# Kernel optimization log

Measured on AMD Instinct MI355X. Metric: run time of the kernel, lower is better.

The kernel has to match this reference:

```python
import jax, jax.numpy as jnp
import numpy as np

N_OBS = 8_000_000
N_CAM = 2_000
N_PTS = 1_000_000


def _rotate_quat(points, qt):
    """Rotate points by unit quaternion qt[...,:4]=(w,x,y,z), then translate by qt[...,4:7]."""
    q = qt[..., :4]
    q = q / jnp.linalg.norm(q, axis=-1, keepdims=True)
    w = q[..., :1]          # [N,1]
    v = q[..., 1:4]         # [N,3]
    # p' = p + 2*v x (v x p + w*p)
    t = jnp.cross(v, points) + w * points
    rotated = points + 2.0 * jnp.cross(v, t)
    return rotated + qt[..., 4:7]


def _project(points, camera_params):
    p = _rotate_quat(points, camera_params[..., :7])          # [N,3]
    proj = -p[..., :2] / p[..., 2:3]                          # perspective divide, [N,2]
    f = camera_params[..., 7:8]
    k1 = camera_params[..., 8:9]
    k2 = camera_params[..., 9:10]
    n = jnp.sum(proj * proj, axis=-1, keepdims=True)          # [N,1]
    r = 1.0 + k1 * n + k2 * n * n                             # radial distortion
    return proj * r * f


def setup_inputs() -> dict:
    key = jax.random.key(0)
    k1, k2, k3, k4, k5 = jax.random.split(key, 5)
    camera_params = jax.random.normal(k1, (N_CAM, 10), dtype=jnp.float32)
    # push translation z away from zero so the perspective divide is well-conditioned
    camera_params = camera_params.at[:, 6].add(5.0)
    points_3d = jax.random.normal(k2, (N_PTS, 3), dtype=jnp.float32)
    points_2d = jax.random.normal(k3, (N_OBS, 2), dtype=jnp.float32)
    camera_indices = jax.random.randint(k4, (N_OBS,), 0, N_CAM, dtype=jnp.int32)
    point_indices = jax.random.randint(k5, (N_OBS,), 0, N_PTS, dtype=jnp.int32)
    return {
        "points_2d": points_2d,
        "camera_indices": camera_indices,
        "point_indices": point_indices,
        "camera_params": camera_params,
        "points_3d": points_3d,
    }


def reference(points_2d, camera_indices, point_indices, camera_params, points_3d):
    pts = points_3d[point_indices]           # gather [N,3]
    cams = camera_params[camera_indices]     # gather [N,10]
    points_proj = _project(pts, cams)        # [N,2]
    return points_proj - points_2d
```

## Files before the change

### kernel.cpp

```cpp
#include <hip/hip_runtime.h>


__device__ __forceinline__ float2 project_one(
    int ci, int pi,
    const float* __restrict__ cams,
    const float* __restrict__ pts,
    float2 obs)
{
    const float2* c2 = reinterpret_cast<const float2*>(cams + (size_t)ci * 10);
    float2 c01 = c2[0];
    float2 c23 = c2[1];
    float2 c45 = c2[2];
    float2 c67 = c2[3];
    float2 c89 = c2[4];

    const float* p = pts + (size_t)pi * 3;
    double px = (double)p[0], py = (double)p[1], pz = (double)p[2];

    double qw = (double)c01.x, qx = (double)c01.y;
    double qy = (double)c23.x, qz = (double)c23.y;

    double nrm2 = qw * qw + qx * qx + qy * qy + qz * qz;
    double s = 1.0 / sqrt(nrm2);
    double w  = qw * s;
    double vx = qx * s, vy = qy * s, vz = qz * s;

    double tx = (vy * pz - vz * py) + w * px;
    double ty = (vz * px - vx * pz) + w * py;
    double tz = (vx * py - vy * px) + w * pz;

    double X = (px + 2.0 * (vy * tz - vz * ty)) + (double)c45.x;
    double Y = (py + 2.0 * (vz * tx - vx * tz)) + (double)c45.y;
    double Z = (pz + 2.0 * (vx * ty - vy * tx)) + (double)c67.x;

    double rz  = 1.0 / Z;
    double prx = -X * rz;
    double pry = -Y * rz;

    double f  = (double)c67.y;
    double k1 = (double)c89.x, k2 = (double)c89.y;

    double nn = prx * prx + pry * pry;
    double r  = 1.0 + k1 * nn + k2 * nn * nn;
    double rf = r * f;

    float2 o;
    o.x = (float)(prx * rf - (double)obs.x);
    o.y = (float)(pry * rf - (double)obs.y);
    return o;
}

__global__ __launch_bounds__(256) void reproj_kernel(
    const float2* __restrict__ p2d,
    const int*    __restrict__ cam_idx,
    const int*    __restrict__ pt_idx,
    const float*  __restrict__ cams,
    const float*  __restrict__ pts,
    float2*       __restrict__ out,
    int n)
{
    int t = blockIdx.x * blockDim.x + threadIdx.x;
    int i = t * 2;
    if (i + 1 < n) {
        int2 ci = *reinterpret_cast<const int2*>(cam_idx + i);
        int2 pi = *reinterpret_cast<const int2*>(pt_idx + i);
        float4 ob = *reinterpret_cast<const float4*>(p2d + i);
        float2 o0 = project_one(ci.x, pi.x, cams, pts, make_float2(ob.x, ob.y));
        float2 o1 = project_one(ci.y, pi.y, cams, pts, make_float2(ob.z, ob.w));
        float4 ov = make_float4(o0.x, o0.y, o1.x, o1.y);
        *reinterpret_cast<float4*>(out + i) = ov;
    } else if (i < n) {
        int ci = cam_idx[i];
        int pi = pt_idx[i];
        float2 ob = p2d[i];
        out[i] = project_one(ci, pi, cams, pts, ob);
    }
}

extern "C" void kernel_launch(void* const* d_in, const int* in_sizes, int n_in,
                              void* d_out, int out_size, void* d_ws, size_t ws_size,
                              hipStream_t stream) {
    const float2* p2d     = (const float2*)d_in[0];
    const int*    cam_idx = (const int*)d_in[1];
    const int*    pt_idx  = (const int*)d_in[2];
    const float*  cams    = (const float*)d_in[3];
    const float*  pts     = (const float*)d_in[4];
    float2*       out     = (float2*)d_out;

    int n = in_sizes[1];

    int threads = 256;
    int elems_per_block = threads * 2;
    int blocks = (n + elems_per_block - 1) / elems_per_block;

    reproj_kernel<<<blocks, threads, 0, stream>>>(p2d, cam_idx, pt_idx, cams, pts, out, n);
}
```

Before: 142.2 us.

## Stage camera table in LDS, repack points to float4, use nontemporal streams

Each 1024-thread block copies the whole 80 KB camera table into shared memory, and the camera gathers then read from LDS. A separate pre-kernel repacks the 3-float points into 16-byte float4 entries in the workspace, so each point gather becomes one vector load. Streaming index, observation and output accesses use nontemporal loads and stores. The trade-off is an extra repack kernel pass over all points, plus a large per-block LDS fill: every block re-reads the full camera table while handling only 2048 observations, and the LDS footprint limits occupancy.

Measured after the change: 155.8 us. 1.1x slower.

```diff
diff --git a/kernel.cpp b/kernel.cpp
--- a/kernel.cpp
+++ b/kernel.cpp
@@ -1,22 +1,34 @@
 #include <hip/hip_runtime.h>
 
 
+typedef __attribute__((ext_vector_type(4))) float f32x4;
+typedef __attribute__((ext_vector_type(2))) int   i32x2;
+
+#define MAX_CAM_WORDS 20000
+
+__global__ void repack_pts_kernel(const float* __restrict__ pts,
+                                  f32x4* __restrict__ out, int npts) {
+    int i = blockIdx.x * blockDim.x + threadIdx.x;
+    if (i < npts) {
+        const float* p = pts + (size_t)i * 3;
+        f32x4 v = {p[0], p[1], p[2], 0.0f};
+        out[i] = v;
+    }
+}
+
 __device__ __forceinline__ float2 project_one(
-    int ci, int pi,
-    const float* __restrict__ cams,
-    const float* __restrict__ pts,
-    float2 obs)
+    const float* lds_cams, int ci,
+    float pxf, float pyf, float pzf,
+    float obsx, float obsy)
 {
-    const float2* c2 = reinterpret_cast<const float2*>(cams + (size_t)ci * 10);
-    float2 c01 = c2[0];
-    float2 c23 = c2[1];
-    float2 c45 = c2[2];
-    float2 c67 = c2[3];
-    float2 c89 = c2[4];
+    const float2* cl = reinterpret_cast<const float2*>(lds_cams + ci * 10);
+    float2 c01 = cl[0];
+    float2 c23 = cl[1];
+    float2 c45 = cl[2];
+    float2 c67 = cl[3];
+    float2 c89 = cl[4];
 
-    const float* p = pts + (size_t)pi * 3;
-    double px = (double)p[0], py = (double)p[1], pz = (double)p[2];
-
+    double px = (double)pxf, py = (double)pyf, pz = (double)pzf;
     double qw = (double)c01.x, qx = (double)c01.y;
     double qy = (double)c23.x, qz = (double)c23.y;
 
@@ -45,53 +57,107 @@
     double rf = r * f;
 
     float2 o;
-    o.x = (float)(prx * rf - (double)obs.x);
-    o.y = (float)(pry * rf - (double)obs.y);
+    o.x = (float)(prx * rf - (double)obsx);
+    o.y = (float)(pry * rf - (double)obsy);
     return o;
 }
 
-__global__ __launch_bounds__(256) void reproj_kernel(
-    const float2* __restrict__ p2d,
+__global__ __launch_bounds__(1024, 8) void reproj_kernel(
+    const f32x4*  __restrict__ p2d4,
     const int*    __restrict__ cam_idx,
     const int*    __restrict__ pt_idx,
     const float*  __restrict__ cams,
-    const float*  __restrict__ pts,
-    float2*       __restrict__ out,
-    int n)
+    const float*  __restrict__ pts_raw,
+    const f32x4*  __restrict__ pts_packed,
+    f32x4*        __restrict__ out4,
+    int n, int ncam_words)
 {
-    int t = blockIdx.x * blockDim.x + threadIdx.x;
-    int i = t * 2;
+    __shared__ float lds_cams[MAX_CAM_WORDS];
+
+    {
+        int nv = ncam_words >> 2;
+        if (nv > (MAX_CAM_WORDS >> 2)) nv = MAX_CAM_WORDS >> 2;
+        const f32x4* src = reinterpret_cast<const f32x4*>(cams);
+        f32x4* dst = reinterpret_cast<f32x4*>(lds_cams);
+        for (int j = threadIdx.x; j < nv; j += blockDim.x)
+            dst[j] = src[j];
+        for (int j = (nv << 2) + threadIdx.x; j < ncam_words && j < MAX_CAM_WORDS;
+             j += blockDim.x)
+            lds_cams[j] = cams[j];
+    }
+    __syncthreads();
+
+    int i = (blockIdx.x * blockDim.x + threadIdx.x) * 2;
     if (i + 1 < n) {
-        int2 ci = *reinterpret_cast<const int2*>(cam_idx + i);
-        int2 pi = *reinterpret_cast<const int2*>(pt_idx + i);
-        float4 ob = *reinterpret_cast<const float4*>(p2d + i);
-        float2 o0 = project_one(ci.x, pi.x, cams, pts, make_float2(ob.x, ob.y));
-        float2 o1 = project_one(ci.y, pi.y, cams, pts, make_float2(ob.z, ob.w));
-        float4 ov = make_float4(o0.x, o0.y, o1.x, o1.y);
-        *reinterpret_cast<float4*>(out + i) = ov;
+        i32x2 ci = __builtin_nontemporal_load(
+            reinterpret_cast<const i32x2*>(cam_idx + i));
+        i32x2 pi = __builtin_nontemporal_load(
+            reinterpret_cast<const i32x2*>(pt_idx + i));
+        f32x4 ob = __builtin_nontemporal_load(p2d4 + (i >> 1));
+
+        float ax, ay, az, bx, by, bz;
+        if (pts_packed) {
+            f32x4 pa = pts_packed[pi.x];
+            f32x4 pb = pts_packed[pi.y];
+            ax = pa.x; ay = pa.y; az = pa.z;
+            bx = pb.x; by = pb.y; bz = pb.z;
+        } else {
+            const float* pA = pts_raw + (size_t)pi.x * 3;
+            const float* pB = pts_raw + (size_t)pi.y * 3;
+            ax = pA[0]; ay = pA[1]; az = pA[2];
+            bx = pB[0]; by = pB[1]; bz = pB[2];
+        }
+
+        float2 o0 = project_one(lds_cams, ci.x, ax, ay, az, ob.x, ob.y);
+        float2 o1 = project_one(lds_cams, ci.y, bx, by, bz, ob.z, ob.w);
+        f32x4 ov = {o0.x, o0.y, o1.x, o1.y};
+        __builtin_nontemporal_store(ov, out4 + (i >> 1));
     } else if (i < n) {
         int ci = cam_idx[i];
         int pi = pt_idx[i];
-        float2 ob = p2d[i];
-        out[i] = project_one(ci, pi, cams, pts, ob);
+        float ax, ay, az;
+        if (pts_packed) {
+            f32x4 pa = pts_packed[pi];
+            ax = pa.x; ay = pa.y; az = pa.z;
+        } else {
+            const float* pA = pts_raw + (size_t)pi * 3;
+            ax = pA[0]; ay = pA[1]; az = pA[2];
+        }
+        const float* p2 = reinterpret_cast<const float*>(p2d4);
+        float2 o = project_one(lds_cams, ci, ax, ay, az,
+                               p2[2 * i], p2[2 * i + 1]);
+        float* po = reinterpret_cast<float*>(out4);
+        po[2 * i]     = o.x;
+        po[2 * i + 1] = o.y;
     }
 }
 
 extern "C" void kernel_launch(void* const* d_in, const int* in_sizes, int n_in,
                               void* d_out, int out_size, void* d_ws, size_t ws_size,
                               hipStream_t stream) {
-    const float2* p2d     = (const float2*)d_in[0];
-    const int*    cam_idx = (const int*)d_in[1];
-    const int*    pt_idx  = (const int*)d_in[2];
-    const float*  cams    = (const float*)d_in[3];
-    const float*  pts     = (const float*)d_in[4];
-    float2*       out     = (float2*)d_out;
+    const float* p2d     = (const float*)d_in[0];
+    const int*   cam_idx = (const int*)d_in[1];
+    const int*   pt_idx  = (const int*)d_in[2];
+    const float* cams    = (const float*)d_in[3];
+    const float* pts     = (const float*)d_in[4];
 
-    int n = in_sizes[1];
+    int n    = in_sizes[1];
+    int ncw  = in_sizes[3];
+    int npts = in_sizes[4] / 3;
 
-    int threads = 256;
-    int elems_per_block = threads * 2;
-    int blocks = (n + elems_per_block - 1) / elems_per_block;
+    f32x4* packed = nullptr;
+    if (ws_size >= (size_t)npts * 16) {
+        packed = (f32x4*)d_ws;
+        int t = 256;
+        int b = (npts + t - 1) / t;
+        repack_pts_kernel<<<b, t, 0, stream>>>(pts, packed, npts);
+    }
 
-    reproj_kernel<<<blocks, threads, 0, stream>>>(p2d, cam_idx, pt_idx, cams, pts, out, n);
+    int threads = 1024;
+    int per_block = threads * 2;
+    int blocks = (n + per_block - 1) / per_block;
+
+    reproj_kernel<<<blocks, threads, 0, stream>>>(
+        (const f32x4*)p2d, cam_idx, pt_idx, cams, pts, packed,
+        (f32x4*)d_out, n, ncw);
 }
```
